# Kernel tuning notes

Hardware: AMD Instinct MI355X
Metric: run time of the kernel (lower is better)

The kernel has to match this reference:

```python
import jax, jax.numpy as jnp
import numpy as np

SELECTOR = jnp.array([29, 49, 79])
N_FINAL = 6
N_EM_ITERS = 10
LOG_2PI = float(np.log(2.0 * np.pi))


def _logdet2(c):
    # log determinant of trailing 2x2 matrices
    return jnp.log(c[..., 0, 0] * c[..., 1, 1] - c[..., 0, 1] * c[..., 1, 0])


def _inv2(c):
    # analytic inverse of trailing 2x2 matrices
    det = c[..., 0, 0] * c[..., 1, 1] - c[..., 0, 1] * c[..., 1, 0]
    inv = jnp.stack([
        jnp.stack([c[..., 1, 1], -c[..., 0, 1]], axis=-1),
        jnp.stack([-c[..., 1, 0], c[..., 0, 0]], axis=-1),
    ], axis=-2)
    return inv / det[..., None, None]


def _initial_state(probas, trajectories):
    B, M = probas.shape
    tsel = trajectories[:, :, SELECTOR, :]                       # [B,M,3,2]
    dots = jnp.einsum('bmtd,bntd->btmn', tsel, tsel)             # [B,3,M,M]
    d1 = jnp.einsum('bmtd,bmtd->btm', tsel, tsel)                # [B,3,M]
    R = jnp.sqrt(d1[:, :, :, None] + d1[:, :, None, :] - 2.0 * dots)
    thr = jnp.quantile(R[:, -1].reshape(B, -1), 0.15, axis=-1)[:, None, None, None]
    adj = (R <= thr).astype(probas.dtype).prod(axis=1)           # [B,M,M]
    worked = jnp.ones((B, M), dtype=probas.dtype)
    bidx = jnp.arange(B)
    idxs = []
    for _ in range(N_FINAL):
        score = (adj * probas[:, None, :]).sum(axis=2) * worked  # [B,M]
        amax = jnp.argmax(score, axis=-1)                        # [B]
        worked = worked * (1.0 - adj[bidx, amax])
        idxs.append(amax)
    return jnp.stack(idxs, axis=1)                               # [B,6]


def _coefficients(cov6, trajectories, traj6, probas6):
    cov6_sel = cov6[:, :, SELECTOR]                              # [B,6,3,2,2]
    prec = _inv2(cov6_sel)                                       # [B,6,3,2,2]
    diff = traj6[:, :, SELECTOR][:, :, None] - trajectories[:, :, SELECTOR][:, None]  # [B,6,M,3,2]
    qform = jnp.einsum('bnmti,bntij,bnmtj->bnmt', diff, prec, diff)
    logdet = _logdet2(cov6_sel)[:, :, None, :]                   # [B,6,1,3]
    pM = jnp.exp((-LOG_2PI - 0.5 * logdet - 0.5 * qform).sum(axis=-1)) + 1e-8  # [B,6,M]
    num = pM * probas6[:, :, None]
    return num / (num.sum(axis=1, keepdims=True) + 1e-8)


def _forward(non_normalized_probas, trajectories, covariance_matrices):
    B = trajectories.shape[0]
    probas = jax.nn.softmax(non_normalized_probas, axis=-1)
    idx = jax.lax.stop_gradient(_initial_state(probas, trajectories))  # [B,6]
    b = jnp.arange(B)[:, None]
    traj6 = trajectories[b, idx]                                 # [B,6,T,2]
    probas6 = jax.nn.softmax(jnp.take_along_axis(non_normalized_probas, idx, axis=1), axis=-1)
    cov6 = covariance_matrices[b, idx]                           # [B,6,T,2,2]
    for _ in range(N_EM_ITERS):
        pM = jax.lax.stop_gradient(_coefficients(cov6, trajectories, traj6, probas6))
        P = probas[:, None, :] * pM                              # [B,6,M]
        probas6 = P.sum(axis=-1)                                 # [B,6]
        traj6 = jnp.einsum('bnm,bmtd->bntd', P, trajectories) / probas6[:, :, None, None]
        diff = traj6[:, :, None] - trajectories[:, None]         # [B,6,M,T,2]
        cov6 = (jnp.einsum('bnm,bmtij->bntij', P, covariance_matrices)
                + jnp.einsum('bnm,bnmti,bnmtj->bntij', P, diff, diff)) / probas6[:, :, None, None, None]
    return probas6, traj6, cov6


def setup_inputs() -> dict:
    key = jax.random.key(0)
    k1, k2, k3 = jax.random.split(key, 3)
    B, M, T = 256, 48, 80
    logits = jax.random.normal(k1, (B, M), dtype=jnp.float32)
    trajectories = jax.random.normal(k2, (B, M, T, 2), dtype=jnp.float32)
    A = 0.3 * jax.random.normal(k3, (B, M, T, 2, 2), dtype=jnp.float32)
    cov = A @ jnp.swapaxes(A, -1, -2) + 0.5 * jnp.eye(2, dtype=jnp.float32)
    return {'non_normalized_probas': logits, 'trajectories': trajectories,
            'covariance_matrices': cov}


def reference(non_normalized_probas, trajectories, covariance_matrices):
    return _forward(non_normalized_probas, trajectories, covariance_matrices)
```

## Files before the change

### kernel.cpp

```cpp
#include <hip/hip_runtime.h>
#include <math.h>

#define BATCH 256
#define M 48
#define T 80
#define NF 6
#define EMIT 10
#define MM (M*M)
#define NW 8
#define LOG2PI 1.8378770664093453f

typedef unsigned int u32;
typedef unsigned long long u64;

#define WGSYNC()     __asm__ __volatile__("s_waitcnt lgkmcnt(0)\ns_barrier" ::: "memory")
#define WGSYNC_ALL() __asm__ __volatile__("s_waitcnt vmcnt(0) lgkmcnt(0)\ns_barrier" ::: "memory")

__global__ __launch_bounds__(512, 1)
void em_kernel(const float* __restrict__ g_logits,
               const float* __restrict__ g_traj,
               const float* __restrict__ g_cov,
               float* __restrict__ g_out)
{
    const int b = blockIdx.x;
    const int tid = threadIdx.x;
    const int lane = tid & 63;
    const int wv = tid >> 6;
    const int SEL[3] = {29, 49, 79};

    __shared__ __align__(16) float s_txy[M*T*2];
    __shared__ __align__(16) float s_cv4[M*T*4];
    __shared__ float s_adj[MM];
    __shared__ float s_logits[M];
    __shared__ float s_probas[M];
    __shared__ float s_tsel[M*6];
    __shared__ float s_d1[M*3];
    __shared__ __align__(16) float s_csel[M*3*4];
    __shared__ __align__(16) float s_Pm[M*8];
    __shared__ __align__(16) float4 s_st[2][NF*3];
    __shared__ __align__(8)  float2 s_t6[2][NF*3];
    __shared__ float s_probas6[2][NF];
    __shared__ int   s_idx[8];
    __shared__ __align__(16) u32 s_hist[NW][4][256];
    __shared__ u32 s_statc[NW], s_statm[NW];

    const float* traj_b = g_traj + (size_t)b*(M*T*2);
    const float* cov_b  = g_cov  + (size_t)b*(M*T*4);

    float myLogit = -1e30f;
    if (lane < M) myLogit = g_logits[b*M + lane];
    float selx[3], sely[3], cc0[3], cc1[3], cc2[3];
    #pragma unroll
    for (int r = 0; r < 3; ++r) {
        int i = lane + r*64;
        if (i < M*3) {
            int m = i/3, tt = i - (i/3)*3;
            float2 xy = ((const float2*)traj_b)[m*T + SEL[tt]];
            float4 cv = ((const float4*)cov_b)[m*T + SEL[tt]];
            selx[r]=xy.x; sely[r]=xy.y; cc0[r]=cv.x; cc1[r]=cv.y; cc2[r]=cv.w;
        }
    }

    __builtin_amdgcn_sched_barrier(0);
    {
        const char* gt = (const char*)traj_b + lane*16;
        char* lt = (char*)s_txy;
        #pragma unroll 2
        for (int k = wv; k < 30; k += NW)
            __builtin_amdgcn_global_load_lds(
                (const __attribute__((address_space(1))) u32*)(gt + k*1024),
                (__attribute__((address_space(3))) u32*)(lt + k*1024), 16, 0, 0);
        const char* gc = (const char*)cov_b + lane*16;
        char* lc = (char*)s_cv4;
        #pragma unroll 2
        for (int k = wv; k < 60; k += NW)
            __builtin_amdgcn_global_load_lds(
                (const __attribute__((address_space(1))) u32*)(gc + k*1024),
                (__attribute__((address_space(3))) u32*)(lc + k*1024), 16, 0, 0);
    }
    __builtin_amdgcn_sched_barrier(0);

    {
        uint4* hz = (uint4*)&s_hist[wv][0][0];
        #pragma unroll
        for (int k = 0; k < 4; ++k) hz[lane + k*64] = make_uint4(0,0,0,0);
    }

    if (lane < M) s_logits[lane] = myLogit;
    #pragma unroll
    for (int r = 0; r < 3; ++r) {
        int i = lane + r*64;
        if (i < M*3) {
            int m = i/3, tt = i - (i/3)*3;
            s_tsel[m*6+tt*2+0] = selx[r];
            s_tsel[m*6+tt*2+1] = sely[r];
            s_d1[i] = selx[r]*selx[r] + sely[r]*sely[r];
            s_csel[i*4+0]=cc0[r]; s_csel[i*4+1]=cc1[r]; s_csel[i*4+2]=cc2[r]; s_csel[i*4+3]=0.f;
        }
    }

    float mx = myLogit;
    #pragma unroll
    for (int off = 32; off; off >>= 1) mx = fmaxf(mx, __shfl_xor(mx, off));
    float pe = (lane < M) ? __expf(myLogit - mx) : 0.f;
    float psum = pe;
    #pragma unroll
    for (int off = 32; off; off >>= 1) psum += __shfl_xor(psum, off);
    const float proba = pe / psum;
    if (lane < M) s_probas[lane] = proba;

    const bool v5 = (tid < MM - 4*512);
    u32 key[5];
    {
        u32* h0 = &s_hist[wv][0][0];
        #pragma unroll
        for (int j = 0; j < 5; ++j) {
            if (j == 4 && !v5) { key[j] = 0xFFFFFFFFu; continue; }
            int e = tid + j*512;
            int m = e/M, n = e - (e/M)*M;
            float dot = s_tsel[m*6+4]*s_tsel[n*6+4] + s_tsel[m*6+5]*s_tsel[n*6+5];
            float v = s_d1[m*3+2] + s_d1[n*3+2] - 2.0f*dot;
            key[j] = __float_as_uint(fmaxf(v, 0.0f));
            atomicAdd(&h0[key[j] >> 24], 1u);
        }
    }

    int target = 345;
    u32 prefix = 0u, pmask = 0u;
    #pragma unroll 1
    for (int r = 0; r < 4; ++r) {
        const int shift = 24 - 8*r;
        if (r) {
            u32* hr = &s_hist[wv][r][0];
            #pragma unroll
            for (int j = 0; j < 5; ++j) {
                if (j == 4 && !v5) continue;
                if ((key[j] & pmask) == prefix)
                    atomicAdd(&hr[(key[j] >> shift) & 255u], 1u);
            }
        }
        WGSYNC();
        u32 hx=0, hy=0, hz=0, hw=0;
        #pragma unroll
        for (int w = 0; w < NW; ++w) {
            uint4 h = ((const uint4*)&s_hist[w][r][0])[lane];
            hx += h.x; hy += h.y; hz += h.z; hw += h.w;
        }
        uint4 hv = make_uint4(hx, hy, hz, hw);
        u32 s4 = hv.x + hv.y + hv.z + hv.w;
        u32 cum = s4;
        #pragma unroll
        for (int off = 1; off < 64; off <<= 1) {
            u32 u = __shfl_up(cum, off);
            if (lane >= off) cum += u;
        }
        u64 bmask = __ballot(cum > (u32)target);
        int g = __builtin_ctzll(bmask);
        int dig = 0; u32 binstart = 0;
        if (lane == g) {
            u32 exc = cum - s4;
            int bi2 = lane*4;
            if (exc + hv.x > (u32)target)      { dig = bi2;   binstart = exc; }
            else { exc += hv.x;
                if (exc + hv.y > (u32)target)  { dig = bi2+1; binstart = exc; }
                else { exc += hv.y;
                    if (exc + hv.z > (u32)target) { dig = bi2+2; binstart = exc; }
                    else { exc += hv.z;            dig = bi2+3; binstart = exc; } } }
        }
        dig = __shfl(dig, g);
        binstart = (u32)__shfl((int)binstart, g);
        target -= (int)binstart;
        prefix |= ((u32)dig) << shift;
        pmask  |= (255u << shift);
    }
    const u32 k1 = prefix;
    const float v1f = sqrtf(__uint_as_float(k1));

    {
        u32 cnt = 0, mng = 0xFFFFFFFFu;
        #pragma unroll
        for (int j = 0; j < 5; ++j) {
            if (j == 4 && !v5) continue;
            if (key[j] <= k1) cnt++;
            else mng = (key[j] < mng) ? key[j] : mng;
        }
        #pragma unroll
        for (int off = 32; off > 0; off >>= 1) {
            cnt += __shfl_down(cnt, off);
            u32 mo = (u32)__shfl_down((int)mng, off);
            mng = (mo < mng) ? mo : mng;
        }
        if (lane == 0) { s_statc[wv] = cnt; s_statm[wv] = mng; }
    }
    WGSYNC();
    float v2f;
    {
        u32 ct = 0, mt = 0xFFFFFFFFu;
        #pragma unroll
        for (int w = 0; w < NW; ++w) {
            ct += s_statc[w];
            if (s_statm[w] < mt) mt = s_statm[w];
        }
        v2f = (ct >= 347u) ? v1f : sqrtf(__uint_as_float(mt));
    }
    const float qi = 0.15f * 2303.0f;
    const float fr = qi - floorf(qi);
    const float thr = v1f*(1.0f - fr) + v2f*fr;

    float dthr;
    {
        u32 ub = __float_as_uint(thr*thr);
        while (sqrtf(__uint_as_float(ub)) > thr) --ub;
        while (sqrtf(__uint_as_float(ub+1u)) <= thr) ++ub;
        dthr = __uint_as_float(ub);
    }

    #pragma unroll
    for (int j = 0; j < 5; ++j) {
        if (j == 4 && !v5) continue;
        int e = tid + j*512;
        int m = e/M, n = e - (e/M)*M;
        float d0 = s_tsel[m*6+0]*s_tsel[n*6+0] + s_tsel[m*6+1]*s_tsel[n*6+1];
        float v0 = fmaxf(s_d1[m*3+0] + s_d1[n*3+0] - 2.0f*d0, 0.0f);
        float d1v = s_tsel[m*6+2]*s_tsel[n*6+2] + s_tsel[m*6+3]*s_tsel[n*6+3];
        float v1 = fmaxf(s_d1[m*3+1] + s_d1[n*3+1] - 2.0f*d1v, 0.0f);
        bool a = (__uint_as_float(key[j]) <= dthr) && (v0 <= dthr) && (v1 <= dthr);
        s_adj[e] = a ? 1.0f : 0.0f;
    }
    WGSYNC();

    const int m = (lane < M) ? lane : (M-1);
    {
        float base = 0.f;
        #pragma unroll
        for (int n = 0; n < M; ++n) base += s_adj[n*M+m] * s_probas[n];
        float worked = 1.f;
        #pragma unroll 1
        for (int k = 0; k < NF; ++k) {
            float sc = (lane < M) ? base*worked : -1.f;
            int bi = lane;
            #pragma unroll
            for (int off = 32; off; off >>= 1) {
                float so = __shfl_down(sc, off);
                int io = __shfl_down(bi, off);
                if (so > sc || (so == sc && io < bi)) { sc = so; bi = io; }
            }
            int amax = __shfl(bi, 0);
            if (lane == 0) s_idx[k] = amax;
            worked *= (1.f - s_adj[amax*M+m]);
        }
    }

    if (lane < NF) {
        float mx6 = -1e30f;
        #pragma unroll
        for (int j = 0; j < NF; ++j) mx6 = fmaxf(mx6, s_logits[s_idx[j]]);
        float sum6 = 0.f;
        #pragma unroll
        for (int j = 0; j < NF; ++j) sum6 += __expf(s_logits[s_idx[j]] - mx6);
        s_probas6[0][lane] = __expf(s_logits[s_idx[lane]] - mx6) / sum6;
    }
    if (lane < NF*3) {
        int n = lane/3, tt = lane - (lane/3)*3;
        int m0 = s_idx[n];
        s_t6[0][lane] = make_float2(s_tsel[m0*6+tt*2+0], s_tsel[m0*6+tt*2+1]);
        float c00 = s_csel[(m0*3+tt)*4+0];
        float c01 = s_csel[(m0*3+tt)*4+1];
        float c11 = s_csel[(m0*3+tt)*4+2];
        float det = c00*c11 - c01*c01;
        float rdet = __fdividef(1.0f, det);
        s_st[0][lane] = make_float4(c11*rdet, -c01*rdet, c00*rdet, __logf(det));
    }

    float tm0=s_tsel[m*6+0], tm1=s_tsel[m*6+1], tm2=s_tsel[m*6+2],
          tm3=s_tsel[m*6+3], tm4=s_tsel[m*6+4], tm5=s_tsel[m*6+5];
    const int gid = tid >> 3;
    const int sub = tid & 7;
    const int gn  = gid/3, gtt = gid - (gid/3)*3;
    const int gslot = (gn < 3) ? gn : gn + 1;

    #pragma unroll 1
    for (int it = 0; it < EMIT; ++it) {
        const int cur = it & 1, nxt = cur ^ 1;
        const float4* stC = s_st[cur];
        const float2* t6C = s_t6[cur];
        const float*  p6C = s_probas6[cur];

        float num[NF]; float den = 1e-8f;
        #pragma unroll
        for (int n = 0; n < NF; ++n) {
            float4 p0 = stC[n*3+0], p1 = stC[n*3+1], p2 = stC[n*3+2];
            float2 a0 = t6C[n*3+0], a1 = t6C[n*3+1], a2 = t6C[n*3+2];
            float lsum = p0.w + p1.w + p2.w;
            float dx0 = a0.x-tm0, dy0 = a0.y-tm1;
            float dx1 = a1.x-tm2, dy1 = a1.y-tm3;
            float dx2 = a2.x-tm4, dy2 = a2.y-tm5;
            float q = p0.x*dx0*dx0 + 2.f*p0.y*dx0*dy0 + p0.z*dy0*dy0
                    + p1.x*dx1*dx1 + 2.f*p1.y*dx1*dy1 + p1.z*dy1*dy1
                    + p2.x*dx2*dx2 + 2.f*p2.y*dx2*dy2 + p2.z*dy2*dy2;
            num[n] = (__expf(-3.f*LOG2PI - 0.5f*lsum - 0.5f*q) + 1e-8f) * p6C[n];
            den += num[n];
        }
        float f = __fdividef(proba, den);
        if (lane < M) {
            *(float4*)&s_Pm[m*8]   = make_float4(num[0]*f, num[1]*f, num[2]*f, 0.f);
            *(float4*)&s_Pm[m*8+4] = make_float4(num[3]*f, num[4]*f, num[5]*f, 0.f);
        }
        if (it == EMIT-1) break;

        if (gid < 18) {
            float SP=0,S1x=0,S1y=0,Sxx=0,Sxy=0,Syy=0,C0=0,C1=0,C2=0;
            #pragma unroll
            for (int k = 0; k < 6; ++k) {
                int mm = sub*6 + k;
                float p = s_Pm[mm*8 + gslot];
                float x = s_tsel[mm*6+gtt*2+0];
                float y = s_tsel[mm*6+gtt*2+1];
                float4 c4 = *(const float4*)&s_csel[(mm*3+gtt)*4];
                SP += p; S1x += p*x; S1y += p*y;
                Sxx += p*x*x; Sxy += p*x*y; Syy += p*y*y;
                C0 += p*c4.x; C1 += p*c4.y; C2 += p*c4.z;
            }
            #define R8(v) { v += __shfl_down(v,4); v += __shfl_down(v,2); v += __shfl_down(v,1); }
            R8(SP) R8(S1x) R8(S1y) R8(Sxx) R8(Sxy) R8(Syy) R8(C0) R8(C1) R8(C2)
            #undef R8
            if (sub == 0) {
                float p6 = SP;
                float tx = __fdividef(S1x, p6), ty = __fdividef(S1y, p6);
                float rp = __fdividef(1.0f, p6);
                float c00 = (C0 + (Sxx - S1x*tx)) * rp;
                float c01 = (C1 + (Sxy - S1x*ty)) * rp;
                float c11 = (C2 + (Syy - S1y*ty)) * rp;
                float det = c00*c11 - c01*c01;
                float rdet = __fdividef(1.0f, det);
                s_st[nxt][gid] = make_float4(c11*rdet, -c01*rdet, c00*rdet, __logf(det));
                s_t6[nxt][gid] = make_float2(tx, ty);
                if (gtt == 0) s_probas6[nxt][gn] = SP;
            }
        }
        WGSYNC();
    }

    WGSYNC_ALL();

    float*  out_p = g_out;
    float2* out_t = (float2*)(g_out + BATCH*NF);
    float4* out_c = (float4*)(g_out + BATCH*NF + BATCH*NF*T*2);
    if (tid < T*NF) {
        int t = tid / NF, n = tid - (tid/NF)*NF;
        int slot = (n < 3) ? n : n + 1;
        float SP=0,S1x=0,S1y=0,Sxx=0,Sxy=0,Syy=0,C00=0,C01=0,C11=0;
        #pragma unroll 4
        for (int mm = 0; mm < M; ++mm) {
            float2 xy = ((const float2*)s_txy)[mm*T + t];
            float4 c4 = ((const float4*)s_cv4)[mm*T + t];
            float p  = s_Pm[mm*8 + slot];
            SP  += p;        S1x += p*xy.x;      S1y += p*xy.y;
            Sxx += p*xy.x*xy.x; Sxy += p*xy.x*xy.y; Syy += p*xy.y*xy.y;
            C00 += p*c4.x;   C01 += p*c4.y;      C11 += p*c4.w;
        }
        float p6 = SP;
        float tx = __fdividef(S1x, p6), ty = __fdividef(S1y, p6);
        float rp = __fdividef(1.0f, p6);
        float c00 = (C00 + (Sxx - S1x*tx)) * rp;
        float c01 = (C01 + (Sxy - S1x*ty)) * rp;
        float c11 = (C11 + (Syy - S1y*ty)) * rp;
        size_t o = (size_t)(b*NF + n)*T + t;
        out_t[o] = make_float2(tx, ty);
        out_c[o] = make_float4(c00, c01, c01, c11);
    }
    if (wv == 0 && lane < NF) {
        int slot = (lane < 3) ? lane : lane + 1;
        float sp = 0.f;
        for (int mm = 0; mm < M; ++mm) sp += s_Pm[mm*8 + slot];
        out_p[b*NF + lane] = sp;
    }
}

extern "C" void kernel_launch(void* const* d_in, const int* in_sizes, int n_in,
                              void* d_out, int out_size, void* d_ws, size_t ws_size,
                              hipStream_t stream) {
    const float* logits = (const float*)d_in[0];
    const float* traj   = (const float*)d_in[1];
    const float* cov    = (const float*)d_in[2];
    float* out = (float*)d_out;
    em_kernel<<<dim3(BATCH), dim3(512), 0, stream>>>(logits, traj, cov, out);
}
```

Measured before the change: 105.5 us.

## Halve workgroup to 256 threads and redistribute per-thread work across phases

Launches 256 threads per batch element instead of 512, with each thread owning 9 pairwise entries instead of 5. The squared distances for the other two selected timesteps are computed once and cached in registers, so the adjacency pass no longer recomputes them. The final M-step is reworked so each thread accumulates two mixture components per timestep, and the per-component mixture weights are written from a wave reduction inside the last EM iteration instead of a serial loop. The aim is to cut barrier cost and redundant work, at the price of more registers per thread and less parallelism in each phase.

```diff
diff --git a/kernel.cpp b/kernel.cpp
--- a/kernel.cpp
+++ b/kernel.cpp
@@ -7,7 +7,8 @@
 #define NF 6
 #define EMIT 10
 #define MM (M*M)
-#define NW 8
+#define NW 4
+#define KPW 9
 #define LOG2PI 1.8378770664093453f
 
 typedef unsigned int u32;
@@ -16,7 +17,7 @@
 #define WGSYNC()     __asm__ __volatile__("s_waitcnt lgkmcnt(0)\ns_barrier" ::: "memory")
 #define WGSYNC_ALL() __asm__ __volatile__("s_waitcnt vmcnt(0) lgkmcnt(0)\ns_barrier" ::: "memory")
 
-__global__ __launch_bounds__(512, 1)
+__global__ __launch_bounds__(256, 1)
 void em_kernel(const float* __restrict__ g_logits,
                const float* __restrict__ g_traj,
                const float* __restrict__ g_cov,
@@ -109,18 +110,21 @@
     const float proba = pe / psum;
     if (lane < M) s_probas[lane] = proba;
 
-    const bool v5 = (tid < MM - 4*512);
-    u32 key[5];
+    u32 key[KPW];
+    float sq0[KPW], sq1[KPW];
     {
         u32* h0 = &s_hist[wv][0][0];
         #pragma unroll
-        for (int j = 0; j < 5; ++j) {
-            if (j == 4 && !v5) { key[j] = 0xFFFFFFFFu; continue; }
-            int e = tid + j*512;
+        for (int j = 0; j < KPW; ++j) {
+            int e = lane + (wv*KPW + j)*64;
             int m = e/M, n = e - (e/M)*M;
-            float dot = s_tsel[m*6+4]*s_tsel[n*6+4] + s_tsel[m*6+5]*s_tsel[n*6+5];
-            float v = s_d1[m*3+2] + s_d1[n*3+2] - 2.0f*dot;
-            key[j] = __float_as_uint(fmaxf(v, 0.0f));
+            float dot2 = s_tsel[m*6+4]*s_tsel[n*6+4] + s_tsel[m*6+5]*s_tsel[n*6+5];
+            float v2 = s_d1[m*3+2] + s_d1[n*3+2] - 2.0f*dot2;
+            key[j] = __float_as_uint(fmaxf(v2, 0.0f));
+            float dot0 = s_tsel[m*6+0]*s_tsel[n*6+0] + s_tsel[m*6+1]*s_tsel[n*6+1];
+            sq0[j] = fmaxf(s_d1[m*3+0] + s_d1[n*3+0] - 2.0f*dot0, 0.0f);
+            float dot1 = s_tsel[m*6+2]*s_tsel[n*6+2] + s_tsel[m*6+3]*s_tsel[n*6+3];
+            sq1[j] = fmaxf(s_d1[m*3+1] + s_d1[n*3+1] - 2.0f*dot1, 0.0f);
             atomicAdd(&h0[key[j] >> 24], 1u);
         }
     }
@@ -133,8 +137,7 @@
         if (r) {
             u32* hr = &s_hist[wv][r][0];
             #pragma unroll
-            for (int j = 0; j < 5; ++j) {
-                if (j == 4 && !v5) continue;
+            for (int j = 0; j < KPW; ++j) {
                 if ((key[j] & pmask) == prefix)
                     atomicAdd(&hr[(key[j] >> shift) & 255u], 1u);
             }
@@ -179,8 +182,7 @@
     {
         u32 cnt = 0, mng = 0xFFFFFFFFu;
         #pragma unroll
-        for (int j = 0; j < 5; ++j) {
-            if (j == 4 && !v5) continue;
+        for (int j = 0; j < KPW; ++j) {
             if (key[j] <= k1) cnt++;
             else mng = (key[j] < mng) ? key[j] : mng;
         }
@@ -216,15 +218,9 @@
     }
 
     #pragma unroll
-    for (int j = 0; j < 5; ++j) {
-        if (j == 4 && !v5) continue;
-        int e = tid + j*512;
-        int m = e/M, n = e - (e/M)*M;
-        float d0 = s_tsel[m*6+0]*s_tsel[n*6+0] + s_tsel[m*6+1]*s_tsel[n*6+1];
-        float v0 = fmaxf(s_d1[m*3+0] + s_d1[n*3+0] - 2.0f*d0, 0.0f);
-        float d1v = s_tsel[m*6+2]*s_tsel[n*6+2] + s_tsel[m*6+3]*s_tsel[n*6+3];
-        float v1 = fmaxf(s_d1[m*3+1] + s_d1[n*3+1] - 2.0f*d1v, 0.0f);
-        bool a = (__uint_as_float(key[j]) <= dthr) && (v0 <= dthr) && (v1 <= dthr);
+    for (int j = 0; j < KPW; ++j) {
+        int e = lane + (wv*KPW + j)*64;
+        bool a = (__uint_as_float(key[j]) <= dthr) && (sq0[j] <= dthr) && (sq1[j] <= dthr);
         s_adj[e] = a ? 1.0f : 0.0f;
     }
     WGSYNC();
@@ -278,6 +274,7 @@
     const int sub = tid & 7;
     const int gn  = gid/3, gtt = gid - (gid/3)*3;
     const int gslot = (gn < 3) ? gn : gn + 1;
+    float*  out_p = g_out;
 
     #pragma unroll 1
     for (int it = 0; it < EMIT; ++it) {
@@ -306,7 +303,18 @@
             *(float4*)&s_Pm[m*8]   = make_float4(num[0]*f, num[1]*f, num[2]*f, 0.f);
             *(float4*)&s_Pm[m*8+4] = make_float4(num[3]*f, num[4]*f, num[5]*f, 0.f);
         }
-        if (it == EMIT-1) break;
+        if (it == EMIT-1) {
+            if (wv == 3) {
+                #pragma unroll
+                for (int n = 0; n < NF; ++n) {
+                    float v = num[n]*f;
+                    #pragma unroll
+                    for (int off = 32; off; off >>= 1) v += __shfl_down(v, off);
+                    if (lane == 0) out_p[b*NF + n] = v;
+                }
+            }
+            break;
+        }
 
         if (gid < 18) {
             float SP=0,S1x=0,S1y=0,Sxx=0,Sxy=0,Syy=0,C0=0,C1=0,C2=0;
@@ -321,9 +329,9 @@
                 Sxx += p*x*x; Sxy += p*x*y; Syy += p*y*y;
                 C0 += p*c4.x; C1 += p*c4.y; C2 += p*c4.z;
             }
-            #define R8(v) { v += __shfl_down(v,4); v += __shfl_down(v,2); v += __shfl_down(v,1); }
-            R8(SP) R8(S1x) R8(S1y) R8(Sxx) R8(Sxy) R8(Syy) R8(C0) R8(C1) R8(C2)
-            #undef R8
+            #define R8_(v) { v += __shfl_down(v,4); v += __shfl_down(v,2); v += __shfl_down(v,1); }
+            R8_(SP) R8_(S1x) R8_(S1y) R8_(Sxx) R8_(Sxy) R8_(Syy) R8_(C0) R8_(C1) R8_(C2)
+            #undef R8_
             if (sub == 0) {
                 float p6 = SP;
                 float tx = __fdividef(S1x, p6), ty = __fdividef(S1y, p6);
@@ -343,37 +351,52 @@
 
     WGSYNC_ALL();
 
-    float*  out_p = g_out;
     float2* out_t = (float2*)(g_out + BATCH*NF);
     float4* out_c = (float4*)(g_out + BATCH*NF + BATCH*NF*T*2);
-    if (tid < T*NF) {
-        int t = tid / NF, n = tid - (tid/NF)*NF;
-        int slot = (n < 3) ? n : n + 1;
-        float SP=0,S1x=0,S1y=0,Sxx=0,Sxy=0,Syy=0,C00=0,C01=0,C11=0;
+    if (lane < 60) {
+        int idx = wv*60 + lane;
+        int t = idx/3, third = idx - (idx/3)*3;
+        int nA = third*2, nB = nA + 1;
+        int slotA = (nA < 3) ? nA : nA + 1;
+        int slotB = (nB < 3) ? nB : nB + 1;
+        float SPa=0,S1xa=0,S1ya=0,Sxxa=0,Sxya=0,Syya=0,C00a=0,C01a=0,C11a=0;
+        float SPb=0,S1xb=0,S1yb=0,Sxxb=0,Sxyb=0,Syyb=0,C00b=0,C01b=0,C11b=0;
         #pragma unroll 4
         for (int mm = 0; mm < M; ++mm) {
             float2 xy = ((const float2*)s_txy)[mm*T + t];
             float4 c4 = ((const float4*)s_cv4)[mm*T + t];
-            float p  = s_Pm[mm*8 + slot];
-            SP  += p;        S1x += p*xy.x;      S1y += p*xy.y;
-            Sxx += p*xy.x*xy.x; Sxy += p*xy.x*xy.y; Syy += p*xy.y*xy.y;
-            C00 += p*c4.x;   C01 += p*c4.y;      C11 += p*c4.w;
-        }
-        float p6 = SP;
-        float tx = __fdividef(S1x, p6), ty = __fdividef(S1y, p6);
-        float rp = __fdividef(1.0f, p6);
-        float c00 = (C00 + (Sxx - S1x*tx)) * rp;
-        float c01 = (C01 + (Sxy - S1x*ty)) * rp;
-        float c11 = (C11 + (Syy - S1y*ty)) * rp;
-        size_t o = (size_t)(b*NF + n)*T + t;
-        out_t[o] = make_float2(tx, ty);
-        out_c[o] = make_float4(c00, c01, c01, c11);
-    }
-    if (wv == 0 && lane < NF) {
-        int slot = (lane < 3) ? lane : lane + 1;
-        float sp = 0.f;
-        for (int mm = 0; mm < M; ++mm) sp += s_Pm[mm*8 + slot];
-        out_p[b*NF + lane] = sp;
+            float pa = s_Pm[mm*8 + slotA];
+            float pb = s_Pm[mm*8 + slotB];
+            float xx = xy.x*xy.x, xyv = xy.x*xy.y, yy = xy.y*xy.y;
+            SPa+=pa; S1xa+=pa*xy.x; S1ya+=pa*xy.y;
+            Sxxa+=pa*xx; Sxya+=pa*xyv; Syya+=pa*yy;
+            C00a+=pa*c4.x; C01a+=pa*c4.y; C11a+=pa*c4.w;
+            SPb+=pb; S1xb+=pb*xy.x; S1yb+=pb*xy.y;
+            Sxxb+=pb*xx; Sxyb+=pb*xyv; Syyb+=pb*yy;
+            C00b+=pb*c4.x; C01b+=pb*c4.y; C11b+=pb*c4.w;
+        }
+        {
+            float p6 = SPa;
+            float tx = __fdividef(S1xa, p6), ty = __fdividef(S1ya, p6);
+            float rp = __fdividef(1.0f, p6);
+            float c00 = (C00a + (Sxxa - S1xa*tx)) * rp;
+            float c01 = (C01a + (Sxya - S1xa*ty)) * rp;
+            float c11 = (C11a + (Syya - S1ya*ty)) * rp;
+            size_t o = (size_t)(b*NF + nA)*T + t;
+            out_t[o] = make_float2(tx, ty);
+            out_c[o] = make_float4(c00, c01, c01, c11);
+        }
+        {
+            float p6 = SPb;
+            float tx = __fdividef(S1xb, p6), ty = __fdividef(S1yb, p6);
+            float rp = __fdividef(1.0f, p6);
+            float c00 = (C00b + (Sxxb - S1xb*tx)) * rp;
+            float c01 = (C01b + (Sxyb - S1xb*ty)) * rp;
+            float c11 = (C11b + (Syyb - S1yb*ty)) * rp;
+            size_t o = (size_t)(b*NF + nB)*T + t;
+            out_t[o] = make_float2(tx, ty);
+            out_c[o] = make_float4(c00, c01, c01, c11);
+        }
     }
 }
 
@@ -384,5 +407,5 @@
     const float* traj   = (const float*)d_in[1];
     const float* cov    = (const float*)d_in[2];
     float* out = (float*)d_out;
-    em_kernel<<<dim3(BATCH), dim3(512), 0, stream>>>(logits, traj, cov, out);
+    em_kernel<<<dim3(BATCH), dim3(256), 0, stream>>>(logits, traj, cov, out);
 }
```

Result: no change. 105.7 us (median of 2 runs) (+0.2%).
